# Performance work log

Hardware: AMD Instinct MI355X
Metric: run time of the kernel (lower is better)

The kernel has to match this reference:

```python
import jax, jax.numpy as jnp
import numpy as np

C = 128
NUM_GROUPS = 32  # min(32, 128 // 4)
EPS = 1e-6


def group_norm(x, gamma, beta):
    N, Cc, H, W = x.shape
    xg = x.reshape(N, NUM_GROUPS, -1)
    mean = xg.mean(axis=-1, keepdims=True)
    var = ((xg - mean) ** 2).mean(axis=-1, keepdims=True)
    xn = ((xg - mean) * jax.lax.rsqrt(var + EPS)).reshape(N, Cc, H, W)
    return xn * gamma[None, :, None, None] + beta[None, :, None, None]


def conv1x1(x, w, b):
    # w: [C_out, C_in], b: [C_out]; 1x1 conv == channel matmul
    return jnp.einsum('nchw,oc->nohw', x, w) + b[None, :, None, None]


def setup_inputs() -> dict:
    key = jax.random.key(0)
    ks = jax.random.split(key, 11)
    s = 1.0 / np.sqrt(C)
    return {
        'x': jax.random.normal(ks[0], (4, C, 64, 64), dtype=jnp.float32),
        'gamma': jnp.ones((C,), jnp.float32),
        'beta': jnp.zeros((C,), jnp.float32),
        'wq': jax.random.normal(ks[1], (C, C), jnp.float32) * s,
        'bq': jnp.zeros((C,), jnp.float32),
        'wk': jax.random.normal(ks[2], (C, C), jnp.float32) * s,
        'bk': jnp.zeros((C,), jnp.float32),
        'wv': jax.random.normal(ks[3], (C, C), jnp.float32) * s,
        'bv': jnp.zeros((C,), jnp.float32),
        'wo': jax.random.normal(ks[4], (C, C), jnp.float32) * s,
        'bo': jnp.zeros((C,), jnp.float32),
    }


def reference(x, gamma, beta, wq, bq, wk, bk, wv, bv, wo, bo):
    N, Cc, H, W = x.shape
    L = H * W
    xn = group_norm(x, gamma, beta)
    q = conv1x1(xn, wq, bq).reshape(N, Cc, L)  # [N,C,L]
    k = conv1x1(xn, wk, bk).reshape(N, Cc, L)
    v = conv1x1(xn, wv, bv).reshape(N, Cc, L)
    scale = 1.0 / jnp.sqrt(jnp.asarray(Cc, x.dtype))
    scores = jnp.einsum('ncl,ncm->nlm', q, k) * scale  # [N,L,L]
    weights = jax.nn.softmax(scores, axis=-1)
    attn = jnp.einsum('nlm,ncm->ncl', weights, v).reshape(N, Cc, H, W)
    return x + conv1x1(attn, wo, bo)
```

## Files before the change

kernel.cpp:

```cpp
#include <hip/hip_runtime.h>
#include <hip/hip_bf16.h>


#define N_B 4
#define C_D 128
#define L_D 4096
#define SPLIT 4
#define KVB 64
#define FSTEPS ((L_D/SPLIT)/KVB)
#define QSCALE (0.08838834764831845f * 1.4426950408889634f)
#define FIXM 16.0f

using f32x4  = __attribute__((ext_vector_type(4))) float;
using f32x16 = __attribute__((ext_vector_type(16))) float;
using bf16x8 = __attribute__((ext_vector_type(8))) short;

static __device__ __forceinline__ unsigned short f2bf(float f){
  return (unsigned short)((__builtin_bit_cast(unsigned int, f) + 0x8000u) >> 16);
}
static __device__ __forceinline__ float bf2f(unsigned short u){
  unsigned int x = ((unsigned int)u) << 16;
  return __builtin_bit_cast(float, x);
}
static __device__ __forceinline__ unsigned int pk2(float a, float b){
  unsigned int ua = __builtin_bit_cast(unsigned int, a) + 0x8000u;
  unsigned int ub = __builtin_bit_cast(unsigned int, b) + 0x8000u;
  return __builtin_amdgcn_perm(ub, ua, 0x07060302u);
}
static __device__ __forceinline__ float exp2a(float x){
  float r; asm("v_exp_f32 %0, %1" : "=v"(r) : "v"(x)); return r;
}
static __device__ __forceinline__ void gll16(const void* g, void* l){
  __builtin_amdgcn_global_load_lds(
      (const __attribute__((address_space(1))) unsigned int*)g,
      (__attribute__((address_space(3))) unsigned int*)l, 16, 0, 0);
}

__global__ __launch_bounds__(256) void gnw_k(
    const float* __restrict__ x, float* __restrict__ stats,
    const float* __restrict__ wq, const float* __restrict__ wk,
    const float* __restrict__ wv, const float* __restrict__ wo,
    unsigned short* __restrict__ wbf)
{
  int b = blockIdx.x, t = threadIdx.x;
  if (b >= 128){
    int b2 = b - 128;
    int mat = b2 >> 4;
    const float* src = (mat == 0) ? wq : (mat == 1) ? wk : (mat == 2) ? wv : wo;
    int off = (b2 & 15) * 1024 + t * 4;
    float4 v = *(const float4*)(src + off);
    *(uint2*)(wbf + mat*16384 + off) = make_uint2(pk2(v.x, v.y), pk2(v.z, v.w));
    return;
  }
  const float4* p = (const float4*)(x + (size_t)b * (4 * L_D));
  float s = 0.f, ss = 0.f;
#pragma unroll
  for (int i = 0; i < 16; ++i){
    float4 v = p[t + i*256];
    s  += v.x + v.y + v.z + v.w;
    ss += v.x*v.x + v.y*v.y + v.z*v.z + v.w*v.w;
  }
#pragma unroll
  for (int off = 32; off > 0; off >>= 1){
    s  += __shfl_down(s, off);
    ss += __shfl_down(ss, off);
  }
  __shared__ float rs4[4], rss4[4];
  if ((t & 63) == 0){ rs4[t>>6] = s; rss4[t>>6] = ss; }
  __syncthreads();
  if (t == 0){
    s  = rs4[0]+rs4[1]+rs4[2]+rs4[3];
    ss = rss4[0]+rss4[1]+rss4[2]+rss4[3];
    float mean = s * (1.f/16384.f);
    float var  = ss * (1.f/16384.f) - mean*mean;
    if (var < 0.f) var = 0.f;
    stats[2*b]   = mean;
    stats[2*b+1] = rsqrtf(var + 1e-6f);
  }
}

__global__ __launch_bounds__(256) void qkv_k(
    const float* __restrict__ x, const float* __restrict__ stats,
    const float* __restrict__ gamma, const float* __restrict__ beta,
    const unsigned short* __restrict__ wbf,
    const float* __restrict__ bq, const float* __restrict__ bk,
    const float* __restrict__ bv,
    unsigned short* __restrict__ q_ws, unsigned short* __restrict__ k_ws,
    unsigned short* __restrict__ v_ws)
{
  __shared__ unsigned short xnT[64][136];
  __shared__ unsigned short qbuf[64][136];

  int t = threadIdx.x, b = blockIdx.x;
  int wi = b >> 8;
  int bt = b & 255;
  int n = bt >> 6, l0 = (bt & 63) * 64;

  {
    int l = t & 63, cq = t >> 6;
#pragma unroll
    for (int it = 0; it < 8; ++it){
      int c0 = cq*4 + it*16;
      int g  = c0 >> 2;
      float mean = stats[(n*32+g)*2];
      float rstd = stats[(n*32+g)*2+1];
      float vv[4];
#pragma unroll
      for (int jj = 0; jj < 4; ++jj){
        int c = c0 + jj;
        float sc = rstd * gamma[c];
        float bs = beta[c] - mean * sc;
        vv[jj] = x[(size_t)(n*C_D + c)*L_D + l0 + l]*sc + bs;
      }
      *(unsigned int*)&xnT[l][c0]   = pk2(vv[0], vv[1]);
      *(unsigned int*)&xnT[l][c0+2] = pk2(vv[2], vv[3]);
    }
  }
  __syncthreads();

  int w = t >> 6, lane = t & 63, u = lane >> 4, l15 = lane & 15;
  int wc = w >> 1, wl = w & 1;
  const unsigned short* W = wbf + wi*16384;
  const float* Bv = (wi == 0) ? bq : (wi == 1) ? bk : bv;

  f32x4 zz = {0.f,0.f,0.f,0.f};
  f32x4 acc[4][2];
#pragma unroll
  for (int ct = 0; ct < 4; ++ct)
#pragma unroll
    for (int lt = 0; lt < 2; ++lt) acc[ct][lt] = zz;

#pragma unroll
  for (int kst = 0; kst < 4; ++kst){
    bf16x8 bfrag[2];
#pragma unroll
    for (int lt = 0; lt < 2; ++lt)
      bfrag[lt] = *(const bf16x8*)&xnT[32*wl + 16*lt + l15][kst*32 + 8*u];
#pragma unroll
    for (int ct = 0; ct < 4; ++ct){
      bf16x8 af = *(const bf16x8*)(W + (size_t)(64*wc + 16*ct + l15)*C_D + kst*32 + 8*u);
#pragma unroll
      for (int lt = 0; lt < 2; ++lt)
        acc[ct][lt] = __builtin_amdgcn_mfma_f32_16x16x32_bf16(af, bfrag[lt], acc[ct][lt], 0, 0, 0);
    }
  }

  if (wi < 2){
    float qs = (wi == 0) ? QSCALE : 1.0f;
#pragma unroll
    for (int ct = 0; ct < 4; ++ct){
      float bias[4];
#pragma unroll
      for (int r = 0; r < 4; ++r) bias[r] = Bv[64*wc + 16*ct + 4*u + r];
#pragma unroll
      for (int lt = 0; lt < 2; ++lt){
        float v0 = (acc[ct][lt][0] + bias[0]) * qs;
        float v1 = (acc[ct][lt][1] + bias[1]) * qs;
        float v2 = (acc[ct][lt][2] + bias[2]) * qs;
        float v3 = (acc[ct][lt][3] + bias[3]) * qs;
        int row = 32*wl + 16*lt + l15;
        int col = 64*wc + 16*ct + 4*u;
        *(unsigned int*)&qbuf[row][col]   = pk2(v0, v1);
        *(unsigned int*)&qbuf[row][col+2] = pk2(v2, v3);
      }
    }
    __syncthreads();
    {
      int l = t >> 2, ch = t & 3;
      unsigned short* dst = ((wi == 0) ? q_ws : k_ws) + (size_t)(n*L_D + l0 + l)*C_D + ch*32;
#pragma unroll
      for (int i = 0; i < 4; ++i)
        *(uint4*)(dst + i*8) = *(const uint4*)&qbuf[l][ch*32 + i*8];
    }
  } else {
    int p16 = (l15 & 3) | ((l15 & 4) << 1) | ((l15 & 8) >> 1);
#pragma unroll
    for (int ct = 0; ct < 4; ++ct){
      float bias[4];
#pragma unroll
      for (int r = 0; r < 4; ++r) bias[r] = Bv[64*wc + 16*ct + 4*u + r];
#pragma unroll
      for (int lt = 0; lt < 2; ++lt)
#pragma unroll
        for (int r = 0; r < 4; ++r){
          int co = 64*wc + 16*ct + 4*u + r;
          v_ws[(size_t)(n*C_D + co)*L_D + l0 + 32*wl + 16*lt + p16] =
              f2bf(acc[ct][lt][r] + bias[r]);
        }
    }
  }
}

__global__ __launch_bounds__(256, 2) void flash_split_k(
    const unsigned short* __restrict__ q_ws, const unsigned short* __restrict__ k_ws,
    const unsigned short* __restrict__ v_ws,
    unsigned short* __restrict__ po_ws, float* __restrict__ md_ws)
{
  __shared__ __align__(16) char shmem[65536];

  int t = threadIdx.x;
  int phys = blockIdx.x;
  int xcd = phys & 7, j = phys >> 3;
  int fkey = xcd*16 + (j & 15);
  int s = j >> 4;
  int n = fkey >> 5, f = fkey & 31;
  int l0 = f * 128;
  int m_base = s * (L_D / SPLIT);
  int w = t >> 6, lane = t & 63, hi = lane >> 5, l31 = lane & 31;
  int lr = lane >> 4, ls = lane & 15;

  bf16x8 qf[8];
  {
    const unsigned short* qrow = q_ws + ((size_t)(n*L_D + l0 + 32*w + l31))*C_D;
#pragma unroll
    for (int kst = 0; kst < 8; ++kst)
      qf[kst] = *(const bf16x8*)(qrow + 16*kst + 8*hi);
  }

  f32x16 zz16;
#pragma unroll
  for (int i = 0; i < 16; ++i) zz16[i] = 0.f;
  f32x16 accO[4];
#pragma unroll
  for (int ct = 0; ct < 4; ++ct) accO[ct] = zz16;
  float rsum = 0.f;

  const unsigned short* kg[4];
  const unsigned short* vg[4];
  int ldof[4];
#pragma unroll
  for (int i = 0; i < 4; ++i){
    int row = 16*w + 4*i + lr;
    int ub = (ls << 4) ^ ((row & 15) << 4);
    kg[i] = k_ws + ((size_t)(n*L_D + m_base + row))*C_D + (ub >> 1);
    int c    = row + ((ub >> 7) << 6);
    int mloc = (ub & 127) >> 1;
    vg[i] = v_ws + ((size_t)(n*C_D + c))*L_D + m_base + mloc;
    ldof[i] = (16*w + 4*i)*256;
  }

  {
#pragma unroll
    for (int i = 0; i < 4; ++i){
      gll16(kg[i], shmem + ldof[i]);
      gll16(vg[i], shmem + 32768 + ldof[i]);
    }
  }
  __syncthreads();

#pragma unroll 2
  for (int step = 0; step < FSTEPS; ++step){
    int cur = step & 1, nxt = cur ^ 1;
    char* kB = shmem + (cur << 14);
    char* vB = shmem + 32768 + (cur << 14);

    if (step + 1 < FSTEPS){
      char* kN = shmem + (nxt << 14);
      char* vN = shmem + 32768 + (nxt << 14);
#pragma unroll
      for (int i = 0; i < 4; ++i){
        gll16(kg[i] + (size_t)(step+1)*KVB*C_D, kN + ldof[i]);
        gll16(vg[i] + (step+1)*KVB,             vN + ldof[i]);
      }
    }

    f32x16 accS[2];
#pragma unroll
    for (int mt = 0; mt < 2; ++mt) accS[mt] = zz16;
    __builtin_amdgcn_s_setprio(1);
#pragma unroll
    for (int mt = 0; mt < 2; ++mt){
      int row = 32*mt + l31;
      bf16x8 afr[8];
#pragma unroll
      for (int kst = 0; kst < 8; ++kst)
        afr[kst] = *(const bf16x8*)(kB + row*256 + ((32*kst + 16*hi) ^ ((row & 15) << 4)));
#pragma unroll
      for (int kst = 0; kst < 8; ++kst)
        accS[mt] = __builtin_amdgcn_mfma_f32_32x32x16_bf16(afr[kst], qf[kst], accS[mt], 0, 0, 0);
    }
    __builtin_amdgcn_s_setprio(0);

    union { unsigned int u[8]; bf16x8 h[2]; } Wm[2];
#pragma unroll
    for (int mt = 0; mt < 2; ++mt){
      float p[16];
#pragma unroll
      for (int r = 0; r < 16; ++r){ p[r] = exp2a(accS[mt][r] - FIXM); rsum += p[r]; }
#pragma unroll
      for (int wd = 0; wd < 8; ++wd) Wm[mt].u[wd] = pk2(p[2*wd], p[2*wd+1]);
    }

    __builtin_amdgcn_s_setprio(1);
#pragma unroll
    for (int sl = 0; sl < 4; ++sl){
      bf16x8 pf = Wm[sl >> 1].h[sl & 1];
      bf16x8 vfr[4];
#pragma unroll
      for (int ct = 0; ct < 4; ++ct){
        int c = 32*ct + l31;
        int vrow = c & 63;
        int lb = ((c >> 6) << 7) + 32*sl + 16*hi;
        vfr[ct] = *(const bf16x8*)(vB + vrow*256 + (lb ^ ((vrow & 15) << 4)));
      }
#pragma unroll
      for (int ct = 0; ct < 4; ++ct)
        accO[ct] = __builtin_amdgcn_mfma_f32_32x32x16_bf16(vfr[ct], pf, accO[ct], 0, 0, 0);
    }
    __builtin_amdgcn_s_setprio(0);
    __syncthreads();
  }

  rsum += __shfl_xor(rsum, 32);

  char* tB = shmem;
  {
    int lloc = 32*w + l31;
    int tsw = (lloc & 15) << 4;
    char* tr = tB + (size_t)lloc*256;
#pragma unroll
    for (int ct = 0; ct < 4; ++ct)
#pragma unroll
      for (int q = 0; q < 4; ++q){
        int cb2 = 64*ct + 16*q + 8*hi;
        *(unsigned int*)(tr + ((cb2    ) ^ tsw)) = pk2(accO[ct][4*q+0], accO[ct][4*q+1]);
        *(unsigned int*)(tr + ((cb2 + 4) ^ tsw)) = pk2(accO[ct][4*q+2], accO[ct][4*q+3]);
      }
  }
  __syncthreads();
  {
    int row2 = t >> 1, hf2 = t & 1;
    size_t pb = ((size_t)((n*32 + f)*SPLIT + s)) * (size_t)(128*128);
    unsigned short* dst = po_ws + pb + (size_t)row2*128 + hf2*64;
    const char* srcr = tB + row2*256;
    int sw2 = (row2 & 15) << 4;
#pragma unroll
    for (int i = 0; i < 8; ++i)
      *(uint4*)(dst + 8*i) = *(const uint4*)(srcr + ((hf2*128 + 16*i) ^ sw2));
  }
  if (lane < 32){
    int lg = 32*w + lane;
    size_t mb2 = ((size_t)((n*32 + f)*SPLIT + s)) * 128;
    md_ws[mb2 + lg] = rsum;
  }
}

__global__ __launch_bounds__(256) void combine_k(
    const unsigned short* __restrict__ po_ws, const float* __restrict__ md_ws,
    const float* __restrict__ x, const unsigned short* __restrict__ wo_bf,
    const float* __restrict__ bo, float* __restrict__ out)
{
  __shared__ __align__(16) char aB[16384];

  int t = threadIdx.x, b = blockIdx.x;
  int xcd = b & 7, j = b >> 3;
  int pair = xcd*8 + (j & 7);
  int quarter = j >> 3;
  int n = pair >> 4, lt256 = pair & 15;
  int lt64 = lt256*4 + quarter;
  int f = lt64 >> 1, loff = (lt64 & 1)*64, l0 = lt64*64;
  size_t pbase = ((size_t)((n*32 + f)*SPLIT)) * (size_t)(128*128);
  size_t mbase = ((size_t)((n*32 + f)*SPLIT)) * 128;

  {
    int l = t >> 2, q = t & 3;
    float Dg = 0.f;
#pragma unroll
    for (int s2 = 0; s2 < SPLIT; ++s2)
      Dg += md_ws[mbase + s2*128 + loff + l];
    float inv = 1.0f / Dg;

    float a[32];
#pragma unroll
    for (int i = 0; i < 32; ++i) a[i] = 0.f;
#pragma unroll
    for (int s2 = 0; s2 < SPLIT; ++s2){
      const uint4* p = (const uint4*)(po_ws + pbase + (size_t)s2*(128*128)
                                      + (size_t)(loff + l)*128 + q*32);
#pragma unroll
      for (int i = 0; i < 4; ++i){
        uint4 uv = p[i];
        unsigned int uu[4] = {uv.x, uv.y, uv.z, uv.w};
#pragma unroll
        for (int j2 = 0; j2 < 4; ++j2){
          a[8*i + 2*j2]     += bf2f((unsigned short)(uu[j2] & 0xffffu));
          a[8*i + 2*j2 + 1] += bf2f((unsigned short)(uu[j2] >> 16));
        }
      }
    }
    char* ar = aB + l*256;
    int asw = (l & 7) << 4;
#pragma unroll
    for (int i = 0; i < 16; ++i){
      int cb = q*64 + 4*i;
      *(unsigned int*)(ar + (cb ^ asw)) = pk2(a[2*i]*inv, a[2*i+1]*inv);
    }
  }
  __syncthreads();

  int w = t >> 6, lane = t & 63, hi = lane >> 5, l31 = lane & 31;
  int lh = w >> 1, ch = w & 1;
  f32x16 acc[2];
#pragma unroll
  for (int ci = 0; ci < 2; ++ci)
#pragma unroll
    for (int i = 0; i < 16; ++i) acc[ci][i] = 0.f;

#pragma unroll
  for (int kst = 0; kst < 8; ++kst){
    int row = 32*lh + l31;
    bf16x8 bfg = *(const bf16x8*)(aB + row*256 + ((32*kst + 16*hi) ^ ((row & 7) << 4)));
#pragma unroll
    for (int ci = 0; ci < 2; ++ci){
      bf16x8 af = *(const bf16x8*)(wo_bf + (size_t)(64*ch + 32*ci + l31)*C_D + 16*kst + 8*hi);
      acc[ci] = __builtin_amdgcn_mfma_f32_32x32x16_bf16(af, bfg, acc[ci], 0, 0, 0);
    }
  }
#pragma unroll
  for (int ci = 0; ci < 2; ++ci)
#pragma unroll
    for (int r = 0; r < 16; ++r){
      int o = 64*ch + 32*ci + (r & 3) + 8*(r >> 2) + 4*hi;
      size_t idx = (size_t)(n*C_D + o)*L_D + l0 + 32*lh + l31;
      out[idx] = x[idx] + bo[o] + acc[ci][r];
    }
}

extern "C" void kernel_launch(void* const* d_in, const int* in_sizes, int n_in,
                              void* d_out, int out_size, void* d_ws, size_t ws_size,
                              hipStream_t stream) {
  const float* x     = (const float*)d_in[0];
  const float* gamma = (const float*)d_in[1];
  const float* beta  = (const float*)d_in[2];
  const float* wq    = (const float*)d_in[3];
  const float* bq    = (const float*)d_in[4];
  const float* wk    = (const float*)d_in[5];
  const float* bk    = (const float*)d_in[6];
  const float* wv    = (const float*)d_in[7];
  const float* bv    = (const float*)d_in[8];
  const float* wo    = (const float*)d_in[9];
  const float* bo    = (const float*)d_in[10];
  float* out = (float*)d_out;

  char* ws = (char*)d_ws;
  float* stats          = (float*)ws;
  unsigned short* q_ws  = (unsigned short*)(ws + 4096);
  unsigned short* k_ws  = q_ws + (size_t)N_B * L_D * C_D;
  unsigned short* v_ws  = k_ws + (size_t)N_B * L_D * C_D;
  unsigned short* po_ws = v_ws + (size_t)N_B * L_D * C_D;
  float* md_ws          = (float*)(po_ws + (size_t)N_B * 32 * SPLIT * 128 * 128);
  unsigned short* wbf   = (unsigned short*)(md_ws + (size_t)N_B * 32 * SPLIT * 128);

  gnw_k<<<192, 256, 0, stream>>>(x, stats, wq, wk, wv, wo, wbf);
  qkv_k<<<768, 256, 0, stream>>>(x, stats, gamma, beta, wbf, bq, bk, bv,
                                 q_ws, k_ws, v_ws);
  flash_split_k<<<512, 256, 0, stream>>>(q_ws, k_ws, v_ws, po_ws, md_ws);
  combine_k<<<256, 256, 0, stream>>>(po_ws, md_ws, x, wbf + 3*16384, bo, out);
}
```

Measured before the change: 73.67 us.

## Software-pipeline QK^T of next KV block with PV of current block

Restructures the flash split-K loop so the QK^T MFMAs for step+1 are interleaved with the PV MFMAs for the current step. The softmax exp work is moved ahead of both, and K is prefetched two steps ahead while V is prefetched one step ahead. The aim is to overlap the exp/pack latency and the LDS reads with matrix-core work inside each step. In exchange it holds two sets of score accumulators in registers, which risks register pressure at 2 waves per SIMD, and the row-sum reduction becomes a tree.

Measured after the change: 74.97 us. No clear change (+1.8%).

```diff
diff --git a/kernel.cpp b/kernel.cpp
--- a/kernel.cpp
+++ b/kernel.cpp
@@ -191,6 +191,70 @@
   }
 }
 
+#define STEPBODY(STEP, SIN, SOUT, CUR, DOQK)                                     \
+  {                                                                              \
+    const int step_ = (STEP);                                                    \
+    if (step_ + 2 < FSTEPS){                                                     \
+      char* kD = shmem + ((CUR) << 14);                                          \
+      _Pragma("unroll")                                                          \
+      for (int i = 0; i < 4; ++i)                                                \
+        gll16(kg[i] + (size_t)(step_+2)*KVB*C_D, kD + ldof[i]);                  \
+    }                                                                            \
+    if (step_ + 1 < FSTEPS){                                                     \
+      char* vD = shmem + 32768 + ((1-(CUR)) << 14);                              \
+      _Pragma("unroll")                                                          \
+      for (int i = 0; i < 4; ++i)                                                \
+        gll16(vg[i] + (step_+1)*KVB, vD + ldof[i]);                              \
+    }                                                                            \
+    union Wu { unsigned int u[8]; bf16x8 h[2]; } Wm[2];                          \
+    _Pragma("unroll")                                                            \
+    for (int mt = 0; mt < 2; ++mt){                                              \
+      float p[16];                                                               \
+      _Pragma("unroll")                                                          \
+      for (int r = 0; r < 16; ++r) p[r] = exp2a(SIN[mt][r] - FIXM);              \
+      float s0 = (p[0]+p[1])+(p[2]+p[3]),   s1 = (p[4]+p[5])+(p[6]+p[7]);        \
+      float s2 = (p[8]+p[9])+(p[10]+p[11]), s3 = (p[12]+p[13])+(p[14]+p[15]);    \
+      rsum += (s0+s1)+(s2+s3);                                                   \
+      _Pragma("unroll")                                                          \
+      for (int wd = 0; wd < 8; ++wd) Wm[mt].u[wd] = pk2(p[2*wd], p[2*wd+1]);     \
+    }                                                                            \
+    bool doQK = (DOQK);                                                          \
+    if (doQK){ SOUT[0] = zz16; SOUT[1] = zz16; }                                 \
+    char* kN = shmem + ((1-(CUR)) << 14);                                        \
+    char* vC = shmem + 32768 + ((CUR) << 14);                                    \
+    __builtin_amdgcn_s_setprio(1);                                               \
+    _Pragma("unroll")                                                            \
+    for (int p2 = 0; p2 < 4; ++p2){                                              \
+      if (doQK){                                                                 \
+        int mt = p2 >> 1, k0 = (p2 & 1) * 4;                                     \
+        int row = 32*mt + l31;                                                   \
+        bf16x8 afr[4];                                                           \
+        _Pragma("unroll")                                                        \
+        for (int kk = 0; kk < 4; ++kk)                                           \
+          afr[kk] = *(const bf16x8*)(kN + row*256 +                              \
+                     ((32*(k0+kk) + 16*hi) ^ ((row & 15) << 4)));                \
+        _Pragma("unroll")                                                        \
+        for (int kk = 0; kk < 4; ++kk)                                           \
+          SOUT[mt] = __builtin_amdgcn_mfma_f32_32x32x16_bf16(                    \
+              afr[kk], qf[k0+kk], SOUT[mt], 0, 0, 0);                            \
+      }                                                                          \
+      bf16x8 pf = Wm[p2 >> 1].h[p2 & 1];                                         \
+      bf16x8 vfr[4];                                                             \
+      _Pragma("unroll")                                                          \
+      for (int ct = 0; ct < 4; ++ct){                                            \
+        int c = 32*ct + l31, vrow = c & 63;                                      \
+        int lb = ((c >> 6) << 7) + 32*p2 + 16*hi;                                \
+        vfr[ct] = *(const bf16x8*)(vC + vrow*256 + (lb ^ ((vrow & 15) << 4)));   \
+      }                                                                          \
+      _Pragma("unroll")                                                          \
+      for (int ct = 0; ct < 4; ++ct)                                             \
+        accO[ct] = __builtin_amdgcn_mfma_f32_32x32x16_bf16(                      \
+            vfr[ct], pf, accO[ct], 0, 0, 0);                                     \
+    }                                                                            \
+    __builtin_amdgcn_s_setprio(0);                                               \
+    __syncthreads();                                                             \
+  }
+
 __global__ __launch_bounds__(256, 2) void flash_split_k(
     const unsigned short* __restrict__ q_ws, const unsigned short* __restrict__ k_ws,
     const unsigned short* __restrict__ v_ws,
@@ -244,29 +308,14 @@
     for (int i = 0; i < 4; ++i){
       gll16(kg[i], shmem + ldof[i]);
       gll16(vg[i], shmem + 32768 + ldof[i]);
-    }
-  }
-  __syncthreads();
-
-#pragma unroll 2
-  for (int step = 0; step < FSTEPS; ++step){
-    int cur = step & 1, nxt = cur ^ 1;
-    char* kB = shmem + (cur << 14);
-    char* vB = shmem + 32768 + (cur << 14);
-
-    if (step + 1 < FSTEPS){
-      char* kN = shmem + (nxt << 14);
-      char* vN = shmem + 32768 + (nxt << 14);
-#pragma unroll
-      for (int i = 0; i < 4; ++i){
-        gll16(kg[i] + (size_t)(step+1)*KVB*C_D, kN + ldof[i]);
-        gll16(vg[i] + (step+1)*KVB,             vN + ldof[i]);
-      }
-    }
-
-    f32x16 accS[2];
-#pragma unroll
-    for (int mt = 0; mt < 2; ++mt) accS[mt] = zz16;
+      gll16(kg[i] + (size_t)KVB*C_D, shmem + 16384 + ldof[i]);
+    }
+  }
+  __syncthreads();
+
+  f32x16 sA[2], sB[2];
+  sA[0] = zz16; sA[1] = zz16;
+  {
     __builtin_amdgcn_s_setprio(1);
 #pragma unroll
     for (int mt = 0; mt < 2; ++mt){
@@ -274,41 +323,18 @@
       bf16x8 afr[8];
 #pragma unroll
       for (int kst = 0; kst < 8; ++kst)
-        afr[kst] = *(const bf16x8*)(kB + row*256 + ((32*kst + 16*hi) ^ ((row & 15) << 4)));
+        afr[kst] = *(const bf16x8*)(shmem + row*256 + ((32*kst + 16*hi) ^ ((row & 15) << 4)));
 #pragma unroll
       for (int kst = 0; kst < 8; ++kst)
-        accS[mt] = __builtin_amdgcn_mfma_f32_32x32x16_bf16(afr[kst], qf[kst], accS[mt], 0, 0, 0);
+        sA[mt] = __builtin_amdgcn_mfma_f32_32x32x16_bf16(afr[kst], qf[kst], sA[mt], 0, 0, 0);
     }
     __builtin_amdgcn_s_setprio(0);
-
-    union { unsigned int u[8]; bf16x8 h[2]; } Wm[2];
-#pragma unroll
-    for (int mt = 0; mt < 2; ++mt){
-      float p[16];
-#pragma unroll
-      for (int r = 0; r < 16; ++r){ p[r] = exp2a(accS[mt][r] - FIXM); rsum += p[r]; }
-#pragma unroll
-      for (int wd = 0; wd < 8; ++wd) Wm[mt].u[wd] = pk2(p[2*wd], p[2*wd+1]);
-    }
-
-    __builtin_amdgcn_s_setprio(1);
-#pragma unroll
-    for (int sl = 0; sl < 4; ++sl){
-      bf16x8 pf = Wm[sl >> 1].h[sl & 1];
-      bf16x8 vfr[4];
-#pragma unroll
-      for (int ct = 0; ct < 4; ++ct){
-        int c = 32*ct + l31;
-        int vrow = c & 63;
-        int lb = ((c >> 6) << 7) + 32*sl + 16*hi;
-        vfr[ct] = *(const bf16x8*)(vB + vrow*256 + (lb ^ ((vrow & 15) << 4)));
-      }
-#pragma unroll
-      for (int ct = 0; ct < 4; ++ct)
-        accO[ct] = __builtin_amdgcn_mfma_f32_32x32x16_bf16(vfr[ct], pf, accO[ct], 0, 0, 0);
-    }
-    __builtin_amdgcn_s_setprio(0);
-    __syncthreads();
+  }
+  __syncthreads();
+
+  for (int e = 0; e < FSTEPS; e += 2){
+    STEPBODY(e,     sA, sB, 0, true)
+    STEPBODY(e + 1, sB, sA, 1, (e + 2 < FSTEPS))
   }
 
   rsum += __shfl_xor(rsum, 32);
```

## Halve KV tile, double split-K to 8, raise flash occupancy

Applied to the files above, without the earlier changes.

The flash kernel now processes 32-key tiles instead of 64, halving shared memory to 32KB and raising launch bounds to 4 blocks per CU. When the workspace is large enough, the KV split factor becomes 8 with 1024 blocks, which gives more parallelism. The cost is more partial-output traffic for combine_k to read and reduce, which now sums 8 partial bf16 tiles. The V shared-memory layout and swizzle were changed to fit the smaller tile.

After: 112.4 us. 52.6% more time.

```diff
diff --git a/kernel.cpp b/kernel.cpp
--- a/kernel.cpp
+++ b/kernel.cpp
@@ -5,9 +5,7 @@
 #define N_B 4
 #define C_D 128
 #define L_D 4096
-#define SPLIT 4
-#define KVB 64
-#define FSTEPS ((L_D/SPLIT)/KVB)
+#define KVB 32
 #define QSCALE (0.08838834764831845f * 1.4426950408889634f)
 #define FIXM 16.0f
 
@@ -191,12 +189,14 @@
   }
 }
 
-__global__ __launch_bounds__(256, 2) void flash_split_k(
+template<int SPL>
+__global__ __launch_bounds__(256, 4) void flash_split_k(
     const unsigned short* __restrict__ q_ws, const unsigned short* __restrict__ k_ws,
     const unsigned short* __restrict__ v_ws,
     unsigned short* __restrict__ po_ws, float* __restrict__ md_ws)
 {
-  __shared__ __align__(16) char shmem[65536];
+  constexpr int FSTEPS = (L_D / SPL) / KVB;
+  __shared__ __align__(16) char shmem[32768];
 
   int t = threadIdx.x;
   int phys = blockIdx.x;
@@ -205,7 +205,7 @@
   int s = j >> 4;
   int n = fkey >> 5, f = fkey & 31;
   int l0 = f * 128;
-  int m_base = s * (L_D / SPLIT);
+  int m_base = s * (L_D / SPL);
   int w = t >> 6, lane = t & 63, hi = lane >> 5, l31 = lane & 31;
   int lr = lane >> 4, ls = lane & 15;
 
@@ -225,83 +225,81 @@
   for (int ct = 0; ct < 4; ++ct) accO[ct] = zz16;
   float rsum = 0.f;
 
-  const unsigned short* kg[4];
-  const unsigned short* vg[4];
-  int ldof[4];
-#pragma unroll
-  for (int i = 0; i < 4; ++i){
-    int row = 16*w + 4*i + lr;
+  const unsigned short* kg[2];
+  const unsigned short* vg[2];
+  int ldof[2];
+#pragma unroll
+  for (int i = 0; i < 2; ++i){
+    int row = 8*w + 4*i + lr;
     int ub = (ls << 4) ^ ((row & 15) << 4);
     kg[i] = k_ws + ((size_t)(n*L_D + m_base + row))*C_D + (ub >> 1);
-    int c    = row + ((ub >> 7) << 6);
-    int mloc = (ub & 127) >> 1;
+    int c    = row + ((ub >> 6) << 5);
+    int mloc = (ub & 63) >> 1;
     vg[i] = v_ws + ((size_t)(n*C_D + c))*L_D + m_base + mloc;
-    ldof[i] = (16*w + 4*i)*256;
-  }
-
-  {
-#pragma unroll
-    for (int i = 0; i < 4; ++i){
+    ldof[i] = (8*w + 4*i)*256;
+  }
+
+  {
+#pragma unroll
+    for (int i = 0; i < 2; ++i){
       gll16(kg[i], shmem + ldof[i]);
-      gll16(vg[i], shmem + 32768 + ldof[i]);
+      gll16(vg[i], shmem + 16384 + ldof[i]);
     }
   }
   __syncthreads();
+
+  int swz = (l31 & 15) << 4;
 
 #pragma unroll 2
   for (int step = 0; step < FSTEPS; ++step){
     int cur = step & 1, nxt = cur ^ 1;
-    char* kB = shmem + (cur << 14);
-    char* vB = shmem + 32768 + (cur << 14);
+    char* kB = shmem + (cur << 13);
+    char* vB = shmem + 16384 + (cur << 13);
 
     if (step + 1 < FSTEPS){
-      char* kN = shmem + (nxt << 14);
-      char* vN = shmem + 32768 + (nxt << 14);
-#pragma unroll
-      for (int i = 0; i < 4; ++i){
+      char* kN = shmem + (nxt << 13);
+      char* vN = shmem + 16384 + (nxt << 13);
+#pragma unroll
+      for (int i = 0; i < 2; ++i){
         gll16(kg[i] + (size_t)(step+1)*KVB*C_D, kN + ldof[i]);
         gll16(vg[i] + (step+1)*KVB,             vN + ldof[i]);
       }
     }
 
-    f32x16 accS[2];
-#pragma unroll
-    for (int mt = 0; mt < 2; ++mt) accS[mt] = zz16;
+    f32x16 accS = zz16;
     __builtin_amdgcn_s_setprio(1);
-#pragma unroll
-    for (int mt = 0; mt < 2; ++mt){
-      int row = 32*mt + l31;
+    {
       bf16x8 afr[8];
 #pragma unroll
       for (int kst = 0; kst < 8; ++kst)
-        afr[kst] = *(const bf16x8*)(kB + row*256 + ((32*kst + 16*hi) ^ ((row & 15) << 4)));
+        afr[kst] = *(const bf16x8*)(kB + l31*256 + ((32*kst + 16*hi) ^ swz));
 #pragma unroll
       for (int kst = 0; kst < 8; ++kst)
-        accS[mt] = __builtin_amdgcn_mfma_f32_32x32x16_bf16(afr[kst], qf[kst], accS[mt], 0, 0, 0);
+        accS = __builtin_amdgcn_mfma_f32_32x32x16_bf16(afr[kst], qf[kst], accS, 0, 0, 0);
     }
     __builtin_amdgcn_s_setprio(0);
 
-    union { unsigned int u[8]; bf16x8 h[2]; } Wm[2];
-#pragma unroll
-    for (int mt = 0; mt < 2; ++mt){
+    union { unsigned int u[8]; bf16x8 h[2]; } Wm;
+    {
       float p[16];
 #pragma unroll
-      for (int r = 0; r < 16; ++r){ p[r] = exp2a(accS[mt][r] - FIXM); rsum += p[r]; }
-#pragma unroll
-      for (int wd = 0; wd < 8; ++wd) Wm[mt].u[wd] = pk2(p[2*wd], p[2*wd+1]);
+      for (int r = 0; r < 16; ++r) p[r] = exp2a(accS[r] - FIXM);
+      float s0 = (p[0]+p[1])+(p[2]+p[3]),   s1 = (p[4]+p[5])+(p[6]+p[7]);
+      float s2 = (p[8]+p[9])+(p[10]+p[11]), s3 = (p[12]+p[13])+(p[14]+p[15]);
+      rsum += (s0+s1)+(s2+s3);
+#pragma unroll
+      for (int wd = 0; wd < 8; ++wd) Wm.u[wd] = pk2(p[2*wd], p[2*wd+1]);
     }
 
     __builtin_amdgcn_s_setprio(1);
 #pragma unroll
-    for (int sl = 0; sl < 4; ++sl){
-      bf16x8 pf = Wm[sl >> 1].h[sl & 1];
+    for (int sl = 0; sl < 2; ++sl){
+      bf16x8 pf = Wm.h[sl];
       bf16x8 vfr[4];
 #pragma unroll
       for (int ct = 0; ct < 4; ++ct){
-        int c = 32*ct + l31;
-        int vrow = c & 63;
-        int lb = ((c >> 6) << 7) + 32*sl + 16*hi;
-        vfr[ct] = *(const bf16x8*)(vB + vrow*256 + (lb ^ ((vrow & 15) << 4)));
+        int lb = ct*64 + 32*sl + 16*hi;
+        vfr[ct] = *(const bf16x8*)(vB + l31*256 + (lb ^ swz));
       }
 #pragma unroll
       for (int ct = 0; ct < 4; ++ct)
@@ -330,7 +328,7 @@
   __syncthreads();
   {
     int row2 = t >> 1, hf2 = t & 1;
-    size_t pb = ((size_t)((n*32 + f)*SPLIT + s)) * (size_t)(128*128);
+    size_t pb = ((size_t)((n*32 + f)*SPL + s)) * (size_t)(128*128);
     unsigned short* dst = po_ws + pb + (size_t)row2*128 + hf2*64;
     const char* srcr = tB + row2*256;
     int sw2 = (row2 & 15) << 4;
@@ -340,11 +338,12 @@
   }
   if (lane < 32){
     int lg = 32*w + lane;
-    size_t mb2 = ((size_t)((n*32 + f)*SPLIT + s)) * 128;
+    size_t mb2 = ((size_t)((n*32 + f)*SPL + s)) * 128;
     md_ws[mb2 + lg] = rsum;
   }
 }
 
+template<int SPL>
 __global__ __launch_bounds__(256) void combine_k(
     const unsigned short* __restrict__ po_ws, const float* __restrict__ md_ws,
     const float* __restrict__ x, const unsigned short* __restrict__ wo_bf,
@@ -359,14 +358,14 @@
   int n = pair >> 4, lt256 = pair & 15;
   int lt64 = lt256*4 + quarter;
   int f = lt64 >> 1, loff = (lt64 & 1)*64, l0 = lt64*64;
-  size_t pbase = ((size_t)((n*32 + f)*SPLIT)) * (size_t)(128*128);
-  size_t mbase = ((size_t)((n*32 + f)*SPLIT)) * 128;
+  size_t pbase = ((size_t)((n*32 + f)*SPL)) * (size_t)(128*128);
+  size_t mbase = ((size_t)((n*32 + f)*SPL)) * 128;
 
   {
     int l = t >> 2, q = t & 3;
     float Dg = 0.f;
 #pragma unroll
-    for (int s2 = 0; s2 < SPLIT; ++s2)
+    for (int s2 = 0; s2 < SPL; ++s2)
       Dg += md_ws[mbase + s2*128 + loff + l];
     float inv = 1.0f / Dg;
 
@@ -374,7 +373,7 @@
 #pragma unroll
     for (int i = 0; i < 32; ++i) a[i] = 0.f;
 #pragma unroll
-    for (int s2 = 0; s2 < SPLIT; ++s2){
+    for (int s2 = 0; s2 < SPL; ++s2){
       const uint4* p = (const uint4*)(po_ws + pbase + (size_t)s2*(128*128)
                                       + (size_t)(loff + l)*128 + q*32);
 #pragma unroll
@@ -442,18 +441,30 @@
   const float* bo    = (const float*)d_in[10];
   float* out = (float*)d_out;
 
+  const size_t qkv_e = (size_t)N_B * L_D * C_D;
+  size_t need8 = 4096 + 3*qkv_e*2
+               + (size_t)N_B*32*8*128*128*2
+               + (size_t)N_B*32*8*128*4
+               + 4*16384*2 + 4096;
+  int spl = (ws_size >= need8) ? 8 : 4;
+
   char* ws = (char*)d_ws;
   float* stats          = (float*)ws;
   unsigned short* q_ws  = (unsigned short*)(ws + 4096);
-  unsigned short* k_ws  = q_ws + (size_t)N_B * L_D * C_D;
-  unsigned short* v_ws  = k_ws + (size_t)N_B * L_D * C_D;
-  unsigned short* po_ws = v_ws + (size_t)N_B * L_D * C_D;
-  float* md_ws          = (float*)(po_ws + (size_t)N_B * 32 * SPLIT * 128 * 128);
-  unsigned short* wbf   = (unsigned short*)(md_ws + (size_t)N_B * 32 * SPLIT * 128);
+  unsigned short* k_ws  = q_ws + qkv_e;
+  unsigned short* v_ws  = k_ws + qkv_e;
+  unsigned short* po_ws = v_ws + qkv_e;
+  float* md_ws          = (float*)(po_ws + (size_t)N_B * 32 * spl * 128 * 128);
+  unsigned short* wbf   = (unsigned short*)(md_ws + (size_t)N_B * 32 * spl * 128);
 
   gnw_k<<<192, 256, 0, stream>>>(x, stats, wq, wk, wv, wo, wbf);
   qkv_k<<<768, 256, 0, stream>>>(x, stats, gamma, beta, wbf, bq, bk, bv,
                                  q_ws, k_ws, v_ws);
-  flash_split_k<<<512, 256, 0, stream>>>(q_ws, k_ws, v_ws, po_ws, md_ws);
-  combine_k<<<256, 256, 0, stream>>>(po_ws, md_ws, x, wbf + 3*16384, bo, out);
-}
+  if (spl == 8){
+    flash_split_k<8><<<1024, 256, 0, stream>>>(q_ws, k_ws, v_ws, po_ws, md_ws);
+    combine_k<8><<<256, 256, 0, stream>>>(po_ws, md_ws, x, wbf + 3*16384, bo, out);
+  } else {
+    flash_split_k<4><<<512, 256, 0, stream>>>(q_ws, k_ws, v_ws, po_ws, md_ws);
+    combine_k<4><<<256, 256, 0, stream>>>(po_ws, md_ws, x, wbf + 3*16384, bo, out);
+  }
+}
```
